# Kernel tuning notes

Measured on AMD Instinct MI355X. Metric: run time of the kernel, lower is better.

## Reference

```python
import jax, jax.numpy as jnp
import numpy as np

VOCAB = 40
CHAR_EMB = 32
CELLS = [512, 1024, 2048]
EMB_SIZE = 512


def _gru_cell(x, h, w_ih, w_hh, b_ih, b_hh):
    # torch GRUCell: gates ordered (r, z, n); w_ih: [3H, In], w_hh: [3H, H]
    gi = x @ w_ih.T + b_ih
    gh = h @ w_hh.T + b_hh
    i_r, i_z, i_n = jnp.split(gi, 3, axis=-1)
    h_r, h_z, h_n = jnp.split(gh, 3, axis=-1)
    r = jax.nn.sigmoid(i_r + h_r)
    zg = jax.nn.sigmoid(i_z + h_z)
    n = jnp.tanh(i_n + r * h_n)
    return (1.0 - zg) * n + zg * h


def setup_inputs() -> dict:
    key = jax.random.key(0)
    ks = iter(jax.random.split(key, 32))

    def glorot(k, shape):
        fan = sum(shape)
        return jax.random.normal(k, shape, jnp.float32) * (2.0 / fan) ** 0.5

    inp = {
        "z": jax.random.normal(next(ks), (64, EMB_SIZE), jnp.float32),
        "emb": glorot(next(ks), (VOCAB, CHAR_EMB)),
        "fc_init_w": glorot(next(ks), (sum(CELLS), EMB_SIZE)),
        "fc_init_b": jnp.zeros((sum(CELLS),), jnp.float32),
        "fc_out_w": glorot(next(ks), (VOCAB, CELLS[-1])),
    }
    in_size = CHAR_EMB
    for li, h in enumerate(CELLS):
        inp[f"w_ih{li}"] = glorot(next(ks), (3 * h, in_size))
        inp[f"w_hh{li}"] = glorot(next(ks), (3 * h, h))
        inp[f"b_ih{li}"] = jnp.zeros((3 * h,), jnp.float32)
        inp[f"b_hh{li}"] = jnp.zeros((3 * h,), jnp.float32)
        in_size = h
    inp["max_len"] = 64
    inp["start_token"] = 1
    return inp


def reference(z, emb, fc_init_w, fc_init_b, fc_out_w,
              w_ih0, w_hh0, b_ih0, b_hh0,
              w_ih1, w_hh1, b_ih1, b_hh1,
              w_ih2, w_hh2, b_ih2, b_hh2,
              max_len, start_token):
    batch = z.shape[0]
    init_states = z @ fc_init_w.T + fc_init_b  # [B, sum(CELLS)]
    splits = np.cumsum(CELLS)[:-1].tolist()
    h0, h1, h2 = jnp.split(init_states, splits, axis=1)
    layers = [(w_ih0, w_hh0, b_ih0, b_hh0),
              (w_ih1, w_hh1, b_ih1, b_hh1),
              (w_ih2, w_hh2, b_ih2, b_hh2)]
    dec0 = jnp.full((batch,), start_token, dtype=jnp.int32)

    def step(carry, _):
        (h0, h1, h2), dec_in = carry
        x = emb[dec_in]  # [B, CHAR_EMB]
        hs = []
        for hprev, (wi, wh, bi, bh) in zip((h0, h1, h2), layers):
            hnew = _gru_cell(x, hprev, wi, wh, bi, bh)
            hs.append(hnew)
            x = hnew
        logits = x @ fc_out_w.T  # [B, VOCAB]
        dec = jnp.argmax(logits, axis=-1).astype(jnp.int32)
        return ((hs[0], hs[1], hs[2]), dec), dec

    _, toks = jax.lax.scan(step, ((h0, h1, h2), dec0), None, length=max_len)
    # toks: [max_len, B] -> [B, max_len, 1] to match torch stack of unsqueezed outputs
    return toks.T[:, :, None].astype(jnp.int64)
```

## Files before the change

kernel.cpp:

```cpp
#include <hip/hip_runtime.h>
#include <math.h>


#define BATCH 64

typedef short bf16x8 __attribute__((ext_vector_type(8)));
typedef float f32x4  __attribute__((ext_vector_type(4)));

__device__ __forceinline__ float sigmoid_f(float x) { return 1.0f / (1.0f + expf(-x)); }

__device__ __forceinline__ void fma4(float& a, const float4 w, const float4 x) {
    a = fmaf(w.x, x.x, a); a = fmaf(w.y, x.y, a);
    a = fmaf(w.z, x.z, a); a = fmaf(w.w, x.w, a);
}

__device__ __forceinline__ unsigned short f2bf(float x) {
    unsigned u = __float_as_uint(x);
    return (unsigned short)((u + 0x7fff + ((u >> 16) & 1)) >> 16);
}
__device__ __forceinline__ float bf2f(unsigned short h) {
    return __uint_as_float(((unsigned)h) << 16);
}
__device__ __forceinline__ void split_bf(float v, short& hi, short& lo) {
    unsigned short h = f2bf(v);
    hi = (short)h;
    lo = (short)f2bf(v - bf2f(h));
}

__device__ __forceinline__ void frag_scatter(short* xhi, short* xlo,
                                             int j, int b, float v) {
    short h, l2; split_bf(v, h, l2);
    const int kblk = j >> 5, off = j & 31;
    const int lp = ((off >> 3) << 4) + (b & 15);
    const int ii = off & 7;
    const int nt = b >> 4;
    const size_t idx = (((size_t)kblk * 4 + nt) * 64 + lp) * 8 + ii;
    xhi[idx] = h; xlo[idx] = l2;
}

__global__ __launch_bounds__(256) void init_misc(
    const float* __restrict__ z, float* __restrict__ zT4,
    int* __restrict__ dec, const int* __restrict__ start_tok)
{
    int tid = blockIdx.x * 256 + threadIdx.x;
    int b  = tid >> 7;
    int k4 = tid & 127;
    ((float4*)zT4)[k4 * 64 + b] = ((const float4*)z)[b * 128 + k4];
    if (tid < BATCH) dec[tid] = start_tok[0];
}

__global__ __launch_bounds__(256) void init_hstate(
    const float* __restrict__ zT4, const float* __restrict__ w,
    const float* __restrict__ bias,
    float* __restrict__ h0, float* __restrict__ h1, float* __restrict__ h2)
{
    const int wave = threadIdx.x >> 6;
    const int b    = threadIdx.x & 63;
    const int r    = blockIdx.x * 4 + wave;
    const float4* w4 = (const float4*)(w + (size_t)r * 512);
    const float4* z4 = (const float4*)zT4;
    float acc = 0.f;
#pragma unroll 8
    for (int k = 0; k < 128; ++k) fma4(acc, w4[k], z4[k * 64 + b]);
    acc += bias[r];
    float* dst; int j;
    if (r < 512)       { dst = h0; j = r; }
    else if (r < 1536) { dst = h1; j = r - 512; }
    else               { dst = h2; j = r - 1536; }
    dst[(((j >> 2) * 64 + b) << 2) + (j & 3)] = acc;
}

__global__ __launch_bounds__(256) void initfrag(
    const float* __restrict__ hT4, short* __restrict__ xhi, short* __restrict__ xlo)
{
    const int gid = blockIdx.x * 256 + threadIdx.x;
    const int j = gid >> 6, b = gid & 63;
    const float v = hT4[(((j >> 2) * 64 + b) << 2) + (j & 3)];
    frag_scatter(xhi, xlo, j, b, v);
}

template<int H, int IN>
__device__ __forceinline__ void wtransform_body(
    const float* __restrict__ w_ih, const float* __restrict__ w_hh,
    short* __restrict__ dhi, short* __restrict__ dlo)
{
    constexpr int KB = (IN + H) / 32;
    const int unit = blockIdx.x * 4 + (threadIdx.x >> 6);
    const int l    = threadIdx.x & 63;
    const int mtile = unit / KB, kblk = unit % KB;
    const int row = mtile * 16 + (l & 15);
    const int kk  = kblk * 32 + ((l >> 4) << 3);
    const float* src = (kk < IN) ? (w_ih + (size_t)row * IN + kk)
                                 : (w_hh + (size_t)row * H + (kk - IN));
    const float4 v0 = *(const float4*)src;
    const float4 v1 = *(const float4*)(src + 4);
    const float vv[8] = {v0.x, v0.y, v0.z, v0.w, v1.x, v1.y, v1.z, v1.w};
    short hi[8], lo[8];
#pragma unroll
    for (int i = 0; i < 8; ++i) split_bf(vv[i], hi[i], lo[i]);
    const size_t base = ((size_t)unit * 64 + l) * 8;
    *(bf16x8*)(dhi + base) = *(const bf16x8*)hi;
    *(bf16x8*)(dlo + base) = *(const bf16x8*)lo;
}
__global__ __launch_bounds__(256) void wtrans_l1(
    const float* __restrict__ a, const float* __restrict__ b,
    short* __restrict__ c, short* __restrict__ d)
{ wtransform_body<1024, 512>(a, b, c, d); }
__global__ __launch_bounds__(256) void wtrans_l2(
    const float* __restrict__ a, const float* __restrict__ b,
    short* __restrict__ c, short* __restrict__ d)
{ wtransform_body<2048, 1024>(a, b, c, d); }

template<int H, int IN>
__device__ __forceinline__ void mfma_gate_body(
    const short* __restrict__ Whi, const short* __restrict__ Wlo,
    const short* __restrict__ XxHi, const short* __restrict__ XxLo,
    const short* __restrict__ XhHi, const short* __restrict__ XhLo,
    float* __restrict__ G)
{
    constexpr int KB  = (IN + H) / 32;
    constexpr int KXB = IN / 32;
    constexpr int GS  = H / 16;
    constexpr int KQ4 = KB / 4;
    constexpr int NG  = KQ4 / 4;

    __shared__ __align__(16) short Ast[2][2][4][2][512];
    __shared__ float red[4][8][64];

    const int tid = threadIdx.x;
    const int wid = tid >> 6;
    const int l   = tid & 63;
    const int nt  = wid & 3;
    const int kh  = wid >> 2;
    const int kq   = blockIdx.x & 1;
    const int rest = blockIdx.x >> 1;
    const int g    = rest / GS;
    const int jb   = rest % GS;

    const int kbase = kq * (KB / 2) + kh * KQ4;
    const size_t abase = ((size_t)(g * GS + jb) * KB) * 512;
    const int pl  = nt & 1;
    const int kl0 = nt >> 1;
    const short* wsrc = (pl ? Wlo : Whi) + abase;

    f32x4 aXa = {0,0,0,0}, aXb = {0,0,0,0}, aHa = {0,0,0,0}, aHb = {0,0,0,0};

    auto stage = [&](int buf, int grp) {
        const int kbb = kbase + grp * 4;
#pragma unroll
        for (int u = 0; u < 2; ++u) {
            const int kloc = kl0 + u * 2;
            const short* ga = wsrc + (size_t)(kbb + kloc) * 512 + (size_t)l * 8;
            __builtin_amdgcn_global_load_lds(
                (const __attribute__((address_space(1))) unsigned int*)ga,
                (__attribute__((address_space(3))) unsigned int*)&Ast[buf][kh][kloc][pl][0],
                16, 0, 0);
        }
    };

    auto comp = [&](int buf, const short* bsH, const short* bsL,
                    f32x4& A1, f32x4& A2) {
#pragma unroll
        for (int i = 0; i < 4; ++i) {
            const bf16x8 ah = *(const bf16x8*)&Ast[buf][kh][i][0][(size_t)l * 8];
            const bf16x8 al = *(const bf16x8*)&Ast[buf][kh][i][1][(size_t)l * 8];
            const bf16x8 bh = *(const bf16x8*)(bsH + (size_t)i * 2048 + (size_t)nt * 512 + (size_t)l * 8);
            const bf16x8 bl = *(const bf16x8*)(bsL + (size_t)i * 2048 + (size_t)nt * 512 + (size_t)l * 8);
            A1 = __builtin_amdgcn_mfma_f32_16x16x32_bf16(ah, bh, A1, 0, 0, 0);
            A2 = __builtin_amdgcn_mfma_f32_16x16x32_bf16(ah, bl, A2, 0, 0, 0);
            A2 = __builtin_amdgcn_mfma_f32_16x16x32_bf16(al, bh, A2, 0, 0, 0);
        }
    };

    stage(0, 0);
    __syncthreads();
#pragma unroll
    for (int grp = 0; grp < NG; ++grp) {
        const int buf = grp & 1;
        if (grp + 1 < NG) stage(buf ^ 1, grp + 1);
        const int kbb = kbase + grp * 4;
        if (kbb < KXB)
            comp(buf, XxHi + (size_t)kbb * 2048, XxLo + (size_t)kbb * 2048, aXa, aXb);
        else
            comp(buf, XhHi + (size_t)(kbb - KXB) * 2048,
                      XhLo + (size_t)(kbb - KXB) * 2048, aHa, aHb);
        __syncthreads();
    }

    float SX[4], SH[4];
#pragma unroll
    for (int t = 0; t < 4; ++t) { SX[t] = aXa[t] + aXb[t]; SH[t] = aHa[t] + aHb[t]; }

    if (kh == 1) {
#pragma unroll
        for (int t = 0; t < 4; ++t) {
            red[nt][t][l]     = SX[t];
            red[nt][4 + t][l] = SH[t];
        }
    }
    __syncthreads();
    if (kh == 0) {
        const int b = nt * 16 + (l & 15);
#pragma unroll
        for (int t = 0; t < 4; ++t) {
            SX[t] += red[nt][t][l];
            SH[t] += red[nt][4 + t][l];
            const int j = jb * 16 + ((l >> 4) << 2) + t;
            if (g == 0)      G[(size_t)((kq * 4 + 0) * H + j) * 64 + b] = SX[t] + SH[t];
            else if (g == 1) G[(size_t)((kq * 4 + 1) * H + j) * 64 + b] = SX[t] + SH[t];
            else {
                G[(size_t)((kq * 4 + 2) * H + j) * 64 + b] = SX[t];
                G[(size_t)((kq * 4 + 3) * H + j) * 64 + b] = SH[t];
            }
        }
    }
}
__global__ __launch_bounds__(512, 2) void mfma_l1(
    const short* __restrict__ a, const short* __restrict__ b,
    const short* __restrict__ c, const short* __restrict__ d,
    const short* __restrict__ e, const short* __restrict__ f,
    float* __restrict__ g)
{ mfma_gate_body<1024, 512>(a, b, c, d, e, f, g); }
__global__ __launch_bounds__(512, 2) void mfma_l2(
    const short* __restrict__ a, const short* __restrict__ b,
    const short* __restrict__ c, const short* __restrict__ d,
    const short* __restrict__ e, const short* __restrict__ f,
    float* __restrict__ g)
{ mfma_gate_body<2048, 1024>(a, b, c, d, e, f, g); }

template<int H>
__device__ __forceinline__ void comb_body(
    const float* __restrict__ G,
    const float* __restrict__ b_ih, const float* __restrict__ b_hh,
    float* __restrict__ hT4, short* __restrict__ xhi, short* __restrict__ xlo)
{
    const int gid = blockIdx.x * 256 + threadIdx.x;
    const int j = gid >> 6, b = gid & 63;
    const size_t o = (size_t)j * 64 + b;
    const size_t P = (size_t)H * 64;
    const float R  = G[0 * P + o] + G[4 * P + o];
    const float Z  = G[1 * P + o] + G[5 * P + o];
    const float NX = G[2 * P + o] + G[6 * P + o];
    const float NH = G[3 * P + o] + G[7 * P + o];
    const float r  = sigmoid_f(R + b_ih[j] + b_hh[j]);
    const float zg = sigmoid_f(Z + b_ih[H + j] + b_hh[H + j]);
    const float n  = tanhf(NX + b_ih[2 * H + j] + r * (NH + b_hh[2 * H + j]));
    const int idx = (((j >> 2) * 64 + b) << 2) + (j & 3);
    const float hp = hT4[idx];
    const float hn = (1.f - zg) * n + zg * hp;
    hT4[idx] = hn;
    frag_scatter(xhi, xlo, j, b, hn);
}
__global__ __launch_bounds__(256) void comb_l1(
    const float* __restrict__ G, const float* __restrict__ bi,
    const float* __restrict__ bh, float* __restrict__ h,
    short* __restrict__ xh, short* __restrict__ xl)
{ comb_body<1024>(G, bi, bh, h, xh, xl); }
__global__ __launch_bounds__(256) void comb_l2(
    const float* __restrict__ G, const float* __restrict__ bi,
    const float* __restrict__ bh, float* __restrict__ h,
    short* __restrict__ xh, short* __restrict__ xl)
{ comb_body<2048>(G, bi, bh, h, xh, xl); }

template<int IN, int H, int C, bool L0>
__device__ __forceinline__ void gru2_body(
    const float* __restrict__ xT4,
    const float* __restrict__ emb, const int* __restrict__ dec,
    const float* __restrict__ hT4_in, float* __restrict__ hT4_out,
    const float* __restrict__ w_ih, const float* __restrict__ w_hh,
    const float* __restrict__ b_ih, const float* __restrict__ b_hh,
    short* __restrict__ xw_hi, short* __restrict__ xw_lo)
{
    constexpr int Q  = (IN + H) / 4;
    constexpr int QX = IN / 4;
    constexpr int QW = Q / 8;

    const int tid  = threadIdx.x;
    const int wave = tid >> 6;
    const int b    = tid & 63;
    const int j0   = blockIdx.x * C;
    const int q0 = wave * QW;
    const int q1 = q0 + QW;

    float accR[C], accZ[C], accNX[C], accNH[C];
#pragma unroll
    for (int c = 0; c < C; ++c) { accR[c]=0.f; accZ[c]=0.f; accNX[c]=0.f; accNH[c]=0.f; }

    {
        const int xe = (q1 < QX) ? q1 : QX;
        if (q0 < xe) {
            const float4* xsrc;
            if (L0) { xsrc = (const float4*)(emb + dec[b] * 32); }
            else    { xsrc = (const float4*)xT4; }
            for (int q = q0; q < xe; ++q) {
                const float4 x = L0 ? xsrc[q] : xsrc[q * 64 + b];
#pragma unroll
                for (int c = 0; c < C; ++c) {
                    const int j = j0 + c;
                    fma4(accR[c],  *(const float4*)(w_ih + ((size_t)j * IN) + 4*q), x);
                    fma4(accZ[c],  *(const float4*)(w_ih + ((size_t)(j + H) * IN) + 4*q), x);
                    fma4(accNX[c], *(const float4*)(w_ih + ((size_t)(j + 2*H) * IN) + 4*q), x);
                }
            }
        }
    }
    {
        const int hs0 = (q0 > QX) ? q0 : QX;
        if (hs0 < q1) {
            const float4* h4 = (const float4*)hT4_in;
#pragma unroll 2
            for (int q = hs0; q < q1; ++q) {
                const int qh = q - QX;
                const float4 hv = h4[qh * 64 + b];
#pragma unroll
                for (int c = 0; c < C; ++c) {
                    const int j = j0 + c;
                    fma4(accR[c],  *(const float4*)(w_hh + ((size_t)j * H) + 4*qh), hv);
                    fma4(accZ[c],  *(const float4*)(w_hh + ((size_t)(j + H) * H) + 4*qh), hv);
                    fma4(accNH[c], *(const float4*)(w_hh + ((size_t)(j + 2*H) * H) + 4*qh), hv);
                }
            }
        }
    }

    __shared__ float red[8][C][4][64];
#pragma unroll
    for (int c = 0; c < C; ++c) {
        red[wave][c][0][b] = accR[c];
        red[wave][c][1][b] = accZ[c];
        red[wave][c][2][b] = accNX[c];
        red[wave][c][3][b] = accNH[c];
    }
    __syncthreads();

    if (tid < C * 64) {
        const int c  = tid >> 6;
        const int bb = tid & 63;
        float R = 0.f, Z = 0.f, NX = 0.f, NH = 0.f;
#pragma unroll
        for (int w = 0; w < 8; ++w) {
            R += red[w][c][0][bb]; Z += red[w][c][1][bb];
            NX += red[w][c][2][bb]; NH += red[w][c][3][bb];
        }
        const int j = j0 + c;
        const float r  = sigmoid_f(R + b_ih[j]     + b_hh[j]);
        const float zg = sigmoid_f(Z + b_ih[j + H] + b_hh[j + H]);
        const float n  = tanhf(NX + b_ih[j + 2 * H] + r * (NH + b_hh[j + 2 * H]));
        const float hp = hT4_in[(((j >> 2) * 64 + bb) << 2) + (j & 3)];
        const float hn = (1.f - zg) * n + zg * hp;
        hT4_out[(((j >> 2) * 64 + bb) << 2) + (j & 3)] = hn;
        if (xw_hi) frag_scatter(xw_hi, xw_lo, j, bb, hn);
    }
}
__global__ __launch_bounds__(512) void gru_l0(
    const float* __restrict__ emb, const int* __restrict__ dec,
    const float* __restrict__ hin, float* __restrict__ hout,
    const float* __restrict__ wi, const float* __restrict__ wh,
    const float* __restrict__ bi, const float* __restrict__ bh,
    short* __restrict__ xh, short* __restrict__ xl)
{ gru2_body<32, 512, 2, true>(nullptr, emb, dec, hin, hout, wi, wh, bi, bh, xh, xl); }
__global__ __launch_bounds__(512) void gru_fb1(
    const float* __restrict__ x, const float* __restrict__ hin, float* __restrict__ hout,
    const float* __restrict__ wi, const float* __restrict__ wh,
    const float* __restrict__ bi, const float* __restrict__ bh)
{ gru2_body<512, 1024, 4, false>(x, nullptr, nullptr, hin, hout, wi, wh, bi, bh, nullptr, nullptr); }
__global__ __launch_bounds__(512) void gru_fb2(
    const float* __restrict__ x, const float* __restrict__ hin, float* __restrict__ hout,
    const float* __restrict__ wi, const float* __restrict__ wh,
    const float* __restrict__ bi, const float* __restrict__ bh)
{ gru2_body<1024, 2048, 4, false>(x, nullptr, nullptr, hin, hout, wi, wh, bi, bh, nullptr, nullptr); }

__global__ __launch_bounds__(512) void out_k(
    const float* __restrict__ h2T4, const float* __restrict__ w_out,
    int* __restrict__ dec, int* __restrict__ out, int s, int max_len)
{
    __shared__ float hs[2048];
    __shared__ float lg[40];
    const int b    = blockIdx.x;
    const int tid  = threadIdx.x;
    const int wave = tid >> 6;
    const int lane = tid & 63;

    const float4* h4 = (const float4*)h2T4;
    ((float4*)hs)[tid] = h4[tid * 64 + b];
    __syncthreads();

    const float4* hs4 = (const float4*)hs;
#pragma unroll
    for (int v = wave * 5; v < wave * 5 + 5; ++v) {
        const float4* w4 = (const float4*)(w_out + (size_t)v * 2048);
        float acc = 0.f;
#pragma unroll
        for (int it = 0; it < 8; ++it) {
            const int k4 = it * 64 + lane;
            fma4(acc, w4[k4], hs4[k4]);
        }
#pragma unroll
        for (int off = 32; off > 0; off >>= 1)
            acc += __shfl_down(acc, off, 64);
        if (lane == 0) lg[v] = acc;
    }
    __syncthreads();

    if (tid == 0) {
        float best = lg[0];
        int bi = 0;
#pragma unroll
        for (int v = 1; v < 40; ++v) {
            const float val = lg[v];
            if (val > best) { best = val; bi = v; }
        }
        dec[b] = bi;
        out[b * max_len + s] = bi;
    }
}

extern "C" void kernel_launch(void* const* d_in, const int* in_sizes, int n_in,
                              void* d_out, int out_size, void* d_ws, size_t ws_size,
                              hipStream_t stream)
{
    const float* z         = (const float*)d_in[0];
    const float* emb       = (const float*)d_in[1];
    const float* fc_init_w = (const float*)d_in[2];
    const float* fc_init_b = (const float*)d_in[3];
    const float* fc_out_w  = (const float*)d_in[4];
    const float* w_ih0 = (const float*)d_in[5];
    const float* w_hh0 = (const float*)d_in[6];
    const float* b_ih0 = (const float*)d_in[7];
    const float* b_hh0 = (const float*)d_in[8];
    const float* w_ih1 = (const float*)d_in[9];
    const float* w_hh1 = (const float*)d_in[10];
    const float* b_ih1 = (const float*)d_in[11];
    const float* b_hh1 = (const float*)d_in[12];
    const float* w_ih2 = (const float*)d_in[13];
    const float* w_hh2 = (const float*)d_in[14];
    const float* b_ih2 = (const float*)d_in[15];
    const float* b_hh2 = (const float*)d_in[16];
    const int* start_tok = (const int*)d_in[18];

    int* out = (int*)d_out;
    const int max_len = out_size / BATCH;
    char* ws = (char*)d_ws;

    const size_t NEED = 103547136;

    if (ws_size >= NEED) {
        short* Wf1hi = (short*)(ws + 0);
        short* Wf1lo = (short*)(ws + 9437184);
        short* Wf2hi = (short*)(ws + 18874368);
        short* Wf2lo = (short*)(ws + 56623104);
        short* XB0hi = (short*)(ws + 94371840);
        short* XB0lo = (short*)(ws + 94437376);
        short* XB1hi[2] = { (short*)(ws + 94502912), (short*)(ws + 94765056) };
        short* XB1lo[2] = { (short*)(ws + 94633984), (short*)(ws + 94896128) };
        short* XB2hi[2] = { (short*)(ws + 95027200), (short*)(ws + 95551488) };
        short* XB2lo[2] = { (short*)(ws + 95289344), (short*)(ws + 95813632) };
        float* h0a = (float*)(ws + 96075776);
        float* h0b = (float*)(ws + 96206848);
        float* h1  = (float*)(ws + 96337920);
        float* h2  = (float*)(ws + 96600064);
        float* zT4 = (float*)(ws + 97124352);
        float* G1  = (float*)(ws + 97255424);
        float* G2  = (float*)(ws + 99352576);
        int*   dec = (int*)  (ws + 103546880);

        wtrans_l1<<<2304, 256, 0, stream>>>(w_ih1, w_hh1, Wf1hi, Wf1lo);
        wtrans_l2<<<9216, 256, 0, stream>>>(w_ih2, w_hh2, Wf2hi, Wf2lo);
        init_misc<<<32, 256, 0, stream>>>(z, zT4, dec, start_tok);
        init_hstate<<<896, 256, 0, stream>>>(zT4, fc_init_w, fc_init_b, h0a, h1, h2);
        initfrag<<<256, 256, 0, stream>>>(h1, XB1hi[0], XB1lo[0]);
        initfrag<<<512, 256, 0, stream>>>(h2, XB2hi[0], XB2lo[0]);

        for (int s = 0; s < max_len; ++s) {
            const int pi = s & 1, po = pi ^ 1;
            const float* h0i = pi ? h0b : h0a;
            float*       h0o = pi ? h0a : h0b;
            gru_l0<<<256, 512, 0, stream>>>(emb, dec, h0i, h0o,
                                            w_ih0, w_hh0, b_ih0, b_hh0,
                                            XB0hi, XB0lo);
            mfma_l1<<<384, 512, 0, stream>>>(Wf1hi, Wf1lo, XB0hi, XB0lo,
                                             XB1hi[pi], XB1lo[pi], G1);
            comb_l1<<<256, 256, 0, stream>>>(G1, b_ih1, b_hh1, h1,
                                             XB1hi[po], XB1lo[po]);
            mfma_l2<<<768, 512, 0, stream>>>(Wf2hi, Wf2lo, XB1hi[po], XB1lo[po],
                                             XB2hi[pi], XB2lo[pi], G2);
            comb_l2<<<512, 256, 0, stream>>>(G2, b_ih2, b_hh2, h2,
                                             XB2hi[po], XB2lo[po]);
            out_k<<<64, 512, 0, stream>>>(h2, fc_out_w, dec, out, s, max_len);
        }
    } else {
        float* zT4    = (float*)(ws + 0);
        float* h0b2[2] = { (float*)(ws + 131072), (float*)(ws + 262144) };
        float* h1b2[2] = { (float*)(ws + 393216), (float*)(ws + 655360) };
        float* h2b2[2] = { (float*)(ws + 917504), (float*)(ws + 1441792) };
        int*   dec    = (int*)(ws + 1966080);

        init_misc<<<32, 256, 0, stream>>>(z, zT4, dec, start_tok);
        init_hstate<<<896, 256, 0, stream>>>(zT4, fc_init_w, fc_init_b,
                                             h0b2[0], h1b2[0], h2b2[0]);
        for (int s = 0; s < max_len; ++s) {
            const int pi = s & 1, po = pi ^ 1;
            gru_l0<<<256, 512, 0, stream>>>(emb, dec, h0b2[pi], h0b2[po],
                                            w_ih0, w_hh0, b_ih0, b_hh0,
                                            nullptr, nullptr);
            gru_fb1<<<256, 512, 0, stream>>>(h0b2[po], h1b2[pi], h1b2[po],
                                             w_ih1, w_hh1, b_ih1, b_hh1);
            gru_fb2<<<512, 512, 0, stream>>>(h1b2[po], h2b2[pi], h2b2[po],
                                             w_ih2, w_hh2, b_ih2, b_hh2);
            out_k<<<64, 512, 0, stream>>>(h2b2[po], fc_out_w, dec, out, s, max_len);
        }
    }
}
```

Measured before the change: 3.210 ms.

## Fuse GRU gate combine into MFMA gate kernels via last-block atomic counter

Removes the separate comb_l1/comb_l2 launches. Each MFMA block increments a per-column-tile atomic counter, and the last of the six contributing blocks computes the GRU nonlinearity, updates h and scatters the bf16 fragments. It also changes the per-stage K group size from 4 to 6 (layer 1) and 8 (layer 2), so there are fewer pipeline iterations. Because a group can now straddle the x/h boundary, the compute loop picks its B source per k-block. The aim is to cut launch overhead and an extra pass over G. In exchange it adds atomics, relies on the tail block seeing the other blocks' G writes through release/acquire, and uses more LDS, which may lower occupancy.

```diff
diff --git a/kernel.cpp b/kernel.cpp
--- a/kernel.cpp
+++ b/kernel.cpp
@@ -79,6 +79,11 @@
     frag_scatter(xhi, xlo, j, b, v);
 }
 
+__global__ void zero_cnt(int* c1, int* c2) {
+    if (threadIdx.x < 64)  c1[threadIdx.x] = 0;
+    if (threadIdx.x < 128) c2[threadIdx.x] = 0;
+}
+
 template<int H, int IN>
 __device__ __forceinline__ void wtransform_body(
     const float* __restrict__ w_ih, const float* __restrict__ w_hh,
@@ -111,21 +116,25 @@
     short* __restrict__ c, short* __restrict__ d)
 { wtransform_body<2048, 1024>(a, b, c, d); }
 
-template<int H, int IN>
+template<int H, int IN, int GB>
 __device__ __forceinline__ void mfma_gate_body(
     const short* __restrict__ Whi, const short* __restrict__ Wlo,
     const short* __restrict__ XxHi, const short* __restrict__ XxLo,
     const short* __restrict__ XhHi, const short* __restrict__ XhLo,
-    float* __restrict__ G)
+    float* __restrict__ G,
+    const float* __restrict__ b_ih, const float* __restrict__ b_hh,
+    float* __restrict__ hT4, short* __restrict__ xhi, short* __restrict__ xlo,
+    int* __restrict__ cnt)
 {
     constexpr int KB  = (IN + H) / 32;
     constexpr int KXB = IN / 32;
     constexpr int GS  = H / 16;
     constexpr int KQ4 = KB / 4;
-    constexpr int NG  = KQ4 / 4;
-
-    __shared__ __align__(16) short Ast[2][2][4][2][512];
+    constexpr int NG  = KQ4 / GB;
+
+    __shared__ __align__(16) short Ast[2][2][GB][2][512];
     __shared__ float red[4][8][64];
+    __shared__ int tailflag;
 
     const int tid = threadIdx.x;
     const int wid = tid >> 6;
@@ -146,9 +155,9 @@
     f32x4 aXa = {0,0,0,0}, aXb = {0,0,0,0}, aHa = {0,0,0,0}, aHb = {0,0,0,0};
 
     auto stage = [&](int buf, int grp) {
-        const int kbb = kbase + grp * 4;
-#pragma unroll
-        for (int u = 0; u < 2; ++u) {
+        const int kbb = kbase + grp * GB;
+#pragma unroll
+        for (int u = 0; u < GB / 2; ++u) {
             const int kloc = kl0 + u * 2;
             const short* ga = wsrc + (size_t)(kbb + kloc) * 512 + (size_t)l * 8;
             __builtin_amdgcn_global_load_lds(
@@ -158,17 +167,28 @@
         }
     };
 
-    auto comp = [&](int buf, const short* bsH, const short* bsL,
-                    f32x4& A1, f32x4& A2) {
-#pragma unroll
-        for (int i = 0; i < 4; ++i) {
+    auto comp = [&](int buf, int grp) {
+        const int kb0 = kbase + grp * GB;
+#pragma unroll
+        for (int i = 0; i < GB; ++i) {
+            const int kbb = kb0 + i;
             const bf16x8 ah = *(const bf16x8*)&Ast[buf][kh][i][0][(size_t)l * 8];
             const bf16x8 al = *(const bf16x8*)&Ast[buf][kh][i][1][(size_t)l * 8];
-            const bf16x8 bh = *(const bf16x8*)(bsH + (size_t)i * 2048 + (size_t)nt * 512 + (size_t)l * 8);
-            const bf16x8 bl = *(const bf16x8*)(bsL + (size_t)i * 2048 + (size_t)nt * 512 + (size_t)l * 8);
-            A1 = __builtin_amdgcn_mfma_f32_16x16x32_bf16(ah, bh, A1, 0, 0, 0);
-            A2 = __builtin_amdgcn_mfma_f32_16x16x32_bf16(ah, bl, A2, 0, 0, 0);
-            A2 = __builtin_amdgcn_mfma_f32_16x16x32_bf16(al, bh, A2, 0, 0, 0);
+            if (kbb < KXB) {
+                const size_t bo = (size_t)kbb * 2048 + (size_t)nt * 512 + (size_t)l * 8;
+                const bf16x8 bh = *(const bf16x8*)(XxHi + bo);
+                const bf16x8 bl = *(const bf16x8*)(XxLo + bo);
+                aXa = __builtin_amdgcn_mfma_f32_16x16x32_bf16(ah, bh, aXa, 0, 0, 0);
+                aXb = __builtin_amdgcn_mfma_f32_16x16x32_bf16(ah, bl, aXb, 0, 0, 0);
+                aXb = __builtin_amdgcn_mfma_f32_16x16x32_bf16(al, bh, aXb, 0, 0, 0);
+            } else {
+                const size_t bo = (size_t)(kbb - KXB) * 2048 + (size_t)nt * 512 + (size_t)l * 8;
+                const bf16x8 bh = *(const bf16x8*)(XhHi + bo);
+                const bf16x8 bl = *(const bf16x8*)(XhLo + bo);
+                aHa = __builtin_amdgcn_mfma_f32_16x16x32_bf16(ah, bh, aHa, 0, 0, 0);
+                aHb = __builtin_amdgcn_mfma_f32_16x16x32_bf16(ah, bl, aHb, 0, 0, 0);
+                aHb = __builtin_amdgcn_mfma_f32_16x16x32_bf16(al, bh, aHb, 0, 0, 0);
+            }
         }
     };
 
@@ -178,12 +198,7 @@
     for (int grp = 0; grp < NG; ++grp) {
         const int buf = grp & 1;
         if (grp + 1 < NG) stage(buf ^ 1, grp + 1);
-        const int kbb = kbase + grp * 4;
-        if (kbb < KXB)
-            comp(buf, XxHi + (size_t)kbb * 2048, XxLo + (size_t)kbb * 2048, aXa, aXb);
-        else
-            comp(buf, XhHi + (size_t)(kbb - KXB) * 2048,
-                      XhLo + (size_t)(kbb - KXB) * 2048, aHa, aHb);
+        comp(buf, grp);
         __syncthreads();
     }
 
@@ -214,53 +229,56 @@
             }
         }
     }
+    __syncthreads();
+
+    if (tid == 0) {
+        const int old = __hip_atomic_fetch_add(&cnt[jb], 1, __ATOMIC_ACQ_REL,
+                                               __HIP_MEMORY_SCOPE_AGENT);
+        tailflag = (old == 5);
+        if (old == 5)
+            __hip_atomic_store(&cnt[jb], 0, __ATOMIC_RELAXED,
+                               __HIP_MEMORY_SCOPE_AGENT);
+    }
+    __syncthreads();
+
+    if (tailflag) {
+        const size_t P = (size_t)H * 64;
+#pragma unroll
+        for (int v = tid; v < 1024; v += 512) {
+            const int j = jb * 16 + (v >> 6);
+            const int b = v & 63;
+            const size_t o = (size_t)j * 64 + b;
+            const float R  = G[0 * P + o] + G[4 * P + o];
+            const float Z  = G[1 * P + o] + G[5 * P + o];
+            const float NX = G[2 * P + o] + G[6 * P + o];
+            const float NH = G[3 * P + o] + G[7 * P + o];
+            const float r  = sigmoid_f(R + b_ih[j] + b_hh[j]);
+            const float zg = sigmoid_f(Z + b_ih[H + j] + b_hh[H + j]);
+            const float n  = tanhf(NX + b_ih[2 * H + j] + r * (NH + b_hh[2 * H + j]));
+            const int idx = (((j >> 2) * 64 + b) << 2) + (j & 3);
+            const float hp = hT4[idx];
+            const float hn = (1.f - zg) * n + zg * hp;
+            hT4[idx] = hn;
+            frag_scatter(xhi, xlo, j, b, hn);
+        }
+    }
 }
 __global__ __launch_bounds__(512, 2) void mfma_l1(
     const short* __restrict__ a, const short* __restrict__ b,
     const short* __restrict__ c, const short* __restrict__ d,
     const short* __restrict__ e, const short* __restrict__ f,
-    float* __restrict__ g)
-{ mfma_gate_body<1024, 512>(a, b, c, d, e, f, g); }
+    float* __restrict__ g, const float* __restrict__ bi,
+    const float* __restrict__ bh, float* __restrict__ h,
+    short* __restrict__ xh, short* __restrict__ xl, int* __restrict__ cnt)
+{ mfma_gate_body<1024, 512, 6>(a, b, c, d, e, f, g, bi, bh, h, xh, xl, cnt); }
 __global__ __launch_bounds__(512, 2) void mfma_l2(
     const short* __restrict__ a, const short* __restrict__ b,
     const short* __restrict__ c, const short* __restrict__ d,
     const short* __restrict__ e, const short* __restrict__ f,
-    float* __restrict__ g)
-{ mfma_gate_body<2048, 1024>(a, b, c, d, e, f, g); }
-
-template<int H>
-__device__ __forceinline__ void comb_body(
-    const float* __restrict__ G,
-    const float* __restrict__ b_ih, const float* __restrict__ b_hh,
-    float* __restrict__ hT4, short* __restrict__ xhi, short* __restrict__ xlo)
-{
-    const int gid = blockIdx.x * 256 + threadIdx.x;
-    const int j = gid >> 6, b = gid & 63;
-    const size_t o = (size_t)j * 64 + b;
-    const size_t P = (size_t)H * 64;
-    const float R  = G[0 * P + o] + G[4 * P + o];
-    const float Z  = G[1 * P + o] + G[5 * P + o];
-    const float NX = G[2 * P + o] + G[6 * P + o];
-    const float NH = G[3 * P + o] + G[7 * P + o];
-    const float r  = sigmoid_f(R + b_ih[j] + b_hh[j]);
-    const float zg = sigmoid_f(Z + b_ih[H + j] + b_hh[H + j]);
-    const float n  = tanhf(NX + b_ih[2 * H + j] + r * (NH + b_hh[2 * H + j]));
-    const int idx = (((j >> 2) * 64 + b) << 2) + (j & 3);
-    const float hp = hT4[idx];
-    const float hn = (1.f - zg) * n + zg * hp;
-    hT4[idx] = hn;
-    frag_scatter(xhi, xlo, j, b, hn);
-}
-__global__ __launch_bounds__(256) void comb_l1(
-    const float* __restrict__ G, const float* __restrict__ bi,
+    float* __restrict__ g, const float* __restrict__ bi,
     const float* __restrict__ bh, float* __restrict__ h,
-    short* __restrict__ xh, short* __restrict__ xl)
-{ comb_body<1024>(G, bi, bh, h, xh, xl); }
-__global__ __launch_bounds__(256) void comb_l2(
-    const float* __restrict__ G, const float* __restrict__ bi,
-    const float* __restrict__ bh, float* __restrict__ h,
-    short* __restrict__ xh, short* __restrict__ xl)
-{ comb_body<2048>(G, bi, bh, h, xh, xl); }
+    short* __restrict__ xh, short* __restrict__ xl, int* __restrict__ cnt)
+{ mfma_gate_body<2048, 1024, 8>(a, b, c, d, e, f, g, bi, bh, h, xh, xl, cnt); }
 
 template<int IN, int H, int C, bool L0>
 __device__ __forceinline__ void gru2_body(
@@ -442,7 +460,7 @@
     const int max_len = out_size / BATCH;
     char* ws = (char*)d_ws;
 
-    const size_t NEED = 103547136;
+    const size_t NEED = 103547904;
 
     if (ws_size >= NEED) {
         short* Wf1hi = (short*)(ws + 0);
@@ -463,6 +481,8 @@
         float* G1  = (float*)(ws + 97255424);
         float* G2  = (float*)(ws + 99352576);
         int*   dec = (int*)  (ws + 103546880);
+        int*   cnt1 = (int*) (ws + 103547136);
+        int*   cnt2 = (int*) (ws + 103547392);
 
         wtrans_l1<<<2304, 256, 0, stream>>>(w_ih1, w_hh1, Wf1hi, Wf1lo);
         wtrans_l2<<<9216, 256, 0, stream>>>(w_ih2, w_hh2, Wf2hi, Wf2lo);
@@ -470,6 +490,7 @@
         init_hstate<<<896, 256, 0, stream>>>(zT4, fc_init_w, fc_init_b, h0a, h1, h2);
         initfrag<<<256, 256, 0, stream>>>(h1, XB1hi[0], XB1lo[0]);
         initfrag<<<512, 256, 0, stream>>>(h2, XB2hi[0], XB2lo[0]);
+        zero_cnt<<<1, 128, 0, stream>>>(cnt1, cnt2);
 
         for (int s = 0; s < max_len; ++s) {
             const int pi = s & 1, po = pi ^ 1;
@@ -479,13 +500,13 @@
                                             w_ih0, w_hh0, b_ih0, b_hh0,
                                             XB0hi, XB0lo);
             mfma_l1<<<384, 512, 0, stream>>>(Wf1hi, Wf1lo, XB0hi, XB0lo,
-                                             XB1hi[pi], XB1lo[pi], G1);
-            comb_l1<<<256, 256, 0, stream>>>(G1, b_ih1, b_hh1, h1,
-                                             XB1hi[po], XB1lo[po]);
+                                             XB1hi[pi], XB1lo[pi], G1,
+                                             b_ih1, b_hh1, h1,
+                                             XB1hi[po], XB1lo[po], cnt1);
             mfma_l2<<<768, 512, 0, stream>>>(Wf2hi, Wf2lo, XB1hi[po], XB1lo[po],
-                                             XB2hi[pi], XB2lo[pi], G2);
-            comb_l2<<<512, 256, 0, stream>>>(G2, b_ih2, b_hh2, h2,
-                                             XB2hi[po], XB2lo[po]);
+                                             XB2hi[pi], XB2lo[pi], G2,
+                                             b_ih2, b_hh2, h2,
+                                             XB2hi[po], XB2lo[po], cnt2);
             out_k<<<64, 512, 0, stream>>>(h2, fc_out_w, dec, out, s, max_len);
         }
     } else {
```

New measurement: 6.028 ms. 87.8% more time.
